# Performance work log

Hardware: AMD Instinct MI355X
Metric: run time of the kernel (lower is better)

The kernel has to match this reference:

```python
import jax, jax.numpy as jnp
import numpy as np
import math

B, L, D, H = 16, 512, 128, 8


def setup_inputs() -> dict:
    key = jax.random.key(0)
    ks = jax.random.split(key, 10)
    xavier = lambda k, shp: jax.random.normal(k, shp, jnp.float32) * math.sqrt(2.0 / (shp[0] + shp[1]))
    inp = {
        "x": jax.random.normal(ks[0], (B, L, D), jnp.float32),
        "W_q": xavier(ks[1], (H * D, D)),
        "b_q": jnp.zeros((H * D,), jnp.float32),
        "W_k": xavier(ks[2], (H * D, D)),
        "b_k": jnp.zeros((H * D,), jnp.float32),
        "W_v": xavier(ks[3], (H * D, D)),
        "b_v": jnp.zeros((H * D,), jnp.float32),
        "W_o": xavier(ks[4], (D, H * D)),
        "b_o": jnp.zeros((D,), jnp.float32),
        "pad_mask": jax.random.randint(ks[5], (B, L, L), 0, 2).astype(bool),
        "batch_size": B,
        "max_len": L,
    }
    return inp


def reference(x, W_q, b_q, W_k, b_k, W_v, b_v, W_o, b_o, pad_mask, batch_size, max_len):
    # project: [B, L, D] -> [B, L, H*D] -> head-major [H*B, L, D]
    def proj(W, b):
        y = jnp.einsum('bld,ed->ble', x, W) + b          # [B, L, H*D]
        y = y.reshape(batch_size, max_len, H, D)
        return y.transpose(2, 0, 1, 3).reshape(H * batch_size, max_len, D)

    q = proj(W_q, b_q)
    k = proj(W_k, b_k)
    v = proj(W_v, b_v)

    scores = jnp.einsum('nqd,nkd->nqk', q, k)            # [H*B, L, L]
    mask = jnp.tile(pad_mask, (H, 1, 1))                 # repeat(n_heads,1,1)
    # faithful quirk: mask BEFORE scaling, softmax over QUERY axis (dim=1)
    scores = jnp.where(mask, -1e9, scores) / math.sqrt(D)
    attn = jax.nn.softmax(scores, axis=1)
    att = jnp.einsum('nqk,nkd->nqd', attn, v)            # [H*B, L, D]
    # faithful quirk: torch .view from (H*B, L, D) to (B, L, H*D)
    att = att.reshape(batch_size, max_len, H * D)
    out = jnp.einsum('ble,de->bld', att, W_o) + b_o      # [B, L, D]
    return out
```

## Files before the change

kernel.cpp:

```cpp
#include <hip/hip_runtime.h>

#define B_  16
#define L_  512
#define D_  128
#define H_  8
#define HD_ 1024
#define NH_ 128
#define M_  8192

typedef unsigned short u16;
typedef __attribute__((ext_vector_type(8))) short s16x8;
typedef __attribute__((ext_vector_type(4))) float f32x4;

__device__ __forceinline__ float bf2f(u16 u) {
    union { unsigned u; float f; } x; x.u = ((unsigned)u) << 16; return x.f;
}
__device__ __forceinline__ u16 f2bf(float f) {
    unsigned u = __float_as_uint(f);
    return (u16)((u + 0x7FFFu + ((u >> 16) & 1u)) >> 16);
}

__device__ __forceinline__ void mfma_bt64(const u16* __restrict__ A, int lda,
                                          const u16* __restrict__ B, int ldb,
                                          int K, int lane, f32x4 acc[4][4]) {
    const int mr = lane & 15, quad = lane >> 4;
    for (int k0 = 0; k0 < K; k0 += 32) {
        s16x8 av[4], bv[4];
#pragma unroll
        for (int i = 0; i < 4; i++)
            av[i] = *(const s16x8*)(A + (size_t)(i * 16 + mr) * lda + k0 + quad * 8);
#pragma unroll
        for (int j = 0; j < 4; j++)
            bv[j] = *(const s16x8*)(B + (size_t)(j * 16 + mr) * ldb + k0 + quad * 8);
#pragma unroll
        for (int i = 0; i < 4; i++)
#pragma unroll
            for (int j = 0; j < 4; j++)
                acc[i][j] = __builtin_amdgcn_mfma_f32_16x16x32_bf16(av[i], bv[j], acc[i][j], 0, 0, 0);
    }
}

__global__ void k0_detect(const unsigned int* __restrict__ pad,
                          const unsigned int* __restrict__ xw,
                          int* __restrict__ flags) {
    __shared__ int sMask, sCnt;
    if (threadIdx.x == 0) { sMask = 0; sCnt = 0; }
    __syncthreads();
    int bad = 0;
#pragma unroll
    for (int i = 0; i < 4; i++) {
        unsigned u = pad[threadIdx.x * 4 + i];
        bad |= (u > 1u) ? 1 : 0;
    }
    int cnt = 0;
#pragma unroll
    for (int i = 0; i < 16; i++) {
        unsigned w = xw[threadIdx.x * 16 + i];
        unsigned e = (w >> 7) & 0xFFu;
        cnt += (e >= 100u && e <= 131u) ? 1 : 0;
    }
    if (bad) atomicOr(&sMask, 1);
    atomicAdd(&sCnt, cnt);
    __syncthreads();
    if (threadIdx.x == 0) {
        flags[0] = (sCnt > 2048) ? 1 : 0;
        flags[1] = sMask;
    }
}

#define PREP_TOT 1576064
__global__ __launch_bounds__(256) void kprep_conv(
    const void* x, const void* Wq, const void* bq, const void* Wk, const void* bk,
    const void* Wv, const void* bv, const void* Wo, const void* bo,
    const int* __restrict__ flags,
    u16* xb, u16* Wqb, u16* Wkb, u16* Wvb, u16* Wob,
    u16* bqb, u16* bkb, u16* bvb, u16* bob) {
    int gid = blockIdx.x * 256 + threadIdx.x;
    if (gid >= PREP_TOT) return;
    const int dt = flags[0];
    const void* src; u16* dst; int off;
    if      (gid < 1048576) { src = x;  dst = xb;  off = gid; }
    else if (gid < 1179648) { src = Wq; dst = Wqb; off = gid - 1048576; }
    else if (gid < 1310720) { src = Wk; dst = Wkb; off = gid - 1179648; }
    else if (gid < 1441792) { src = Wv; dst = Wvb; off = gid - 1310720; }
    else if (gid < 1572864) { src = Wo; dst = Wob; off = gid - 1441792; }
    else if (gid < 1573888) { src = bq; dst = bqb; off = gid - 1572864; }
    else if (gid < 1574912) { src = bk; dst = bkb; off = gid - 1573888; }
    else if (gid < 1575936) { src = bv; dst = bvb; off = gid - 1574912; }
    else                    { src = bo; dst = bob; off = gid - 1575936; }
    dst[off] = dt ? ((const u16*)src)[off] : f2bf(((const float*)src)[off]);
}

__global__ __launch_bounds__(256) void kprep_mask(const void* __restrict__ pad,
                                                  const int* __restrict__ flags,
                                                  unsigned* __restrict__ mb) {
    int w = blockIdx.x * 256 + threadIdx.x;
    size_t base = (size_t)w * 32;
    unsigned m = 0;
    if (flags[1]) {
        const unsigned char* p = (const unsigned char*)pad;
#pragma unroll
        for (int b = 0; b < 32; b++) m |= (p[base + b] ? 1u : 0u) << b;
    } else {
        const int* p = (const int*)pad;
#pragma unroll
        for (int b = 0; b < 32; b++) m |= (p[base + b] ? 1u : 0u) << b;
    }
    mb[w] = m;
}

__global__ __launch_bounds__(256) void k1_proj(
    const u16* __restrict__ xb,
    const u16* __restrict__ Wqb, const u16* __restrict__ Wkb, const u16* __restrict__ Wvb,
    const u16* __restrict__ bqb, const u16* __restrict__ bkb, const u16* __restrict__ bvb,
    u16* __restrict__ qb, u16* __restrict__ kb, u16* __restrict__ vtb) {
    const int h  = blockIdx.x;
    const int m0 = blockIdx.y * 128;
    const int z  = blockIdx.z;
    const u16* W    = (z == 0) ? Wqb : (z == 1) ? Wkb : Wvb;
    const u16* bias = (z == 0) ? bqb : (z == 1) ? bkb : bvb;

    const int lane = threadIdx.x & 63, wave = threadIdx.x >> 6;
    const int wr = wave >> 1, wc = wave & 1;
    const int mr = lane & 15, quad = lane >> 4;

    f32x4 acc[4][4];
#pragma unroll
    for (int i = 0; i < 4; i++)
#pragma unroll
        for (int j = 0; j < 4; j++) acc[i][j] = (f32x4){0.f, 0.f, 0.f, 0.f};

    mfma_bt64(xb + (size_t)(m0 + wr * 64) * D_, D_,
              W + (size_t)(h * 128 + wc * 64) * D_, D_, D_, lane, acc);

    __shared__ __align__(16) u16 T[128][144];
#pragma unroll
    for (int i = 0; i < 4; i++)
#pragma unroll
        for (int j = 0; j < 4; j++) {
            int col = wc * 64 + j * 16 + mr;
            float bv_ = bf2f(bias[h * 128 + col]);
#pragma unroll
            for (int r = 0; r < 4; r++)
                T[wr * 64 + i * 16 + quad * 4 + r][col] = f2bf(acc[i][j][r] + bv_);
        }
    __syncthreads();

    const int bb = m0 >> 9, l0 = m0 & 511;
    const int t = threadIdx.x;
    if (z < 2) {
        u16* out = z ? kb : qb;
        int row = t >> 1, c0 = (t & 1) * 64;
        u16* dst = out + ((size_t)(h * B_ + bb) * L_ + l0 + row) * D_ + c0;
#pragma unroll
        for (int c = 0; c < 64; c += 8)
            *(uint4*)(dst + c) = *(const uint4*)&T[row][c0 + c];
    } else {
        int d = t >> 1, lc0 = (t & 1) * 64;
        u16* dst = vtb + ((size_t)(h * B_ + bb) * D_ + d) * L_ + l0 + lc0;
#pragma unroll
        for (int c = 0; c < 64; c += 8) {
            u16 tmp[8];
#pragma unroll
            for (int s = 0; s < 8; s++) tmp[s] = T[lc0 + c + s][d];
            *(uint4*)(dst + c) = *(const uint4*)tmp;
        }
    }
}

__global__ __launch_bounds__(256) void k2_scores(
    const u16* __restrict__ qb, const u16* __restrict__ kb,
    const unsigned* __restrict__ mbits,
    u16* __restrict__ sb, float* __restrict__ linv) {
    const int k0g = blockIdx.x * 128;
    const int n   = blockIdx.y;
    const int bb  = n & (B_ - 1);
    const int lane = threadIdx.x & 63, wave = threadIdx.x >> 6;
    const int wr = wave >> 1, wc = wave & 1;
    const int mr = lane & 15, quad = lane >> 4;
    const float rs = 0.08838834764831845f;

    __shared__ __align__(16) u16 T[128][144];
    __shared__ float CS[2][128];

    const u16* Abase = qb + (size_t)n * L_ * D_;
    const u16* Bbase = kb + (size_t)n * L_ * D_ + (size_t)(k0g + wc * 64) * D_;

    float colsum[4] = {0.f, 0.f, 0.f, 0.f};
    for (int qt = 0; qt < 4; qt++) {
        f32x4 acc[4][4];
#pragma unroll
        for (int i = 0; i < 4; i++)
#pragma unroll
            for (int j = 0; j < 4; j++) acc[i][j] = (f32x4){0.f, 0.f, 0.f, 0.f};

        mfma_bt64(Abase + (size_t)(qt * 128 + wr * 64) * D_, D_, Bbase, D_, D_, lane, acc);

#pragma unroll
        for (int i = 0; i < 4; i++)
#pragma unroll
            for (int j = 0; j < 4; j++) {
                int kc = k0g + wc * 64 + j * 16 + mr;
#pragma unroll
                for (int r = 0; r < 4; r++) {
                    int ql = wr * 64 + i * 16 + quad * 4 + r;
                    int q  = qt * 128 + ql;
                    unsigned w = mbits[((size_t)(bb << 9) + q) * 16 + (kc >> 5)];
                    float s = ((w >> (kc & 31)) & 1u) ? -1e9f : acc[i][j][r];
                    float e = __expf(s * rs);
                    colsum[j] += e;
                    T[ql][wc * 64 + j * 16 + mr] = f2bf(e);
                }
            }
        __syncthreads();
        {
            int t = threadIdx.x, row = t >> 1, c0 = (t & 1) * 64;
            u16* dst = sb + ((size_t)n * L_ + qt * 128 + row) * L_ + k0g + c0;
#pragma unroll
            for (int c = 0; c < 64; c += 8)
                *(uint4*)(dst + c) = *(const uint4*)&T[row][c0 + c];
        }
        __syncthreads();
    }
#pragma unroll
    for (int j = 0; j < 4; j++) {
        colsum[j] += __shfl_xor(colsum[j], 16);
        colsum[j] += __shfl_xor(colsum[j], 32);
    }
    if (quad == 0) {
#pragma unroll
        for (int j = 0; j < 4; j++) CS[wr][wc * 64 + j * 16 + mr] = colsum[j];
    }
    __syncthreads();
    if (threadIdx.x < 128)
        linv[(size_t)n * L_ + k0g + threadIdx.x] =
            1.0f / (CS[0][threadIdx.x] + CS[1][threadIdx.x]);
}

__global__ __launch_bounds__(256) void k3_vscale(u16* __restrict__ vtb,
                                                 const float* __restrict__ linv) {
    int idx = blockIdx.x * 256 + threadIdx.x;
    int n = idx >> 13;
    int rem = idx & 8191;
    int d = rem >> 6;
    int kg = (rem & 63) << 3;
    u16* p = vtb + ((size_t)n * D_ + d) * L_ + kg;
    uint4 v = *(const uint4*)p;
    float lv[8];
    *(float4*)&lv[0] = *(const float4*)(linv + (size_t)n * L_ + kg);
    *(float4*)&lv[4] = *(const float4*)(linv + (size_t)n * L_ + kg + 4);
    u16* u = (u16*)&v;
#pragma unroll
    for (int s = 0; s < 8; s++) u[s] = f2bf(bf2f(u[s]) * lv[s]);
    *(uint4*)p = v;
}

__global__ __launch_bounds__(256) void k4_av(
    const u16* __restrict__ sb, const u16* __restrict__ vtb,
    u16* __restrict__ att) {
    const int q0 = blockIdx.x * 128;
    const int n  = blockIdx.y;
    const int lane = threadIdx.x & 63, wave = threadIdx.x >> 6;
    const int wr = wave >> 1, wc = wave & 1;
    const int mr = lane & 15, quad = lane >> 4;

    f32x4 acc[4][4];
#pragma unroll
    for (int i = 0; i < 4; i++)
#pragma unroll
        for (int j = 0; j < 4; j++) acc[i][j] = (f32x4){0.f, 0.f, 0.f, 0.f};

    mfma_bt64(sb + ((size_t)n * L_ + q0 + wr * 64) * L_, L_,
              vtb + ((size_t)n * D_ + wc * 64) * L_, L_, L_, lane, acc);

    __shared__ __align__(16) u16 T[128][144];
#pragma unroll
    for (int i = 0; i < 4; i++)
#pragma unroll
        for (int j = 0; j < 4; j++) {
            int col = wc * 64 + j * 16 + mr;
#pragma unroll
            for (int r = 0; r < 4; r++)
                T[wr * 64 + i * 16 + quad * 4 + r][col] = f2bf(acc[i][j][r]);
        }
    __syncthreads();
    int t = threadIdx.x, row = t >> 1, c0 = (t & 1) * 64;
    u16* dst = att + ((size_t)n * L_ + q0 + row) * D_ + c0;
#pragma unroll
    for (int c = 0; c < 64; c += 8)
        *(uint4*)(dst + c) = *(const uint4*)&T[row][c0 + c];
}

__global__ __launch_bounds__(128) void k5_out(
    const u16* __restrict__ att, const u16* __restrict__ Wob,
    const u16* __restrict__ bob, const int* __restrict__ flags,
    void* __restrict__ out) {
    const int dt = flags[0];
    const int m0 = blockIdx.x * 64;
    const int lane = threadIdx.x & 63, wc = threadIdx.x >> 6;
    const int mr = lane & 15, quad = lane >> 4;

    f32x4 acc[4][4];
#pragma unroll
    for (int i = 0; i < 4; i++)
#pragma unroll
        for (int j = 0; j < 4; j++) acc[i][j] = (f32x4){0.f, 0.f, 0.f, 0.f};

    mfma_bt64(att + (size_t)m0 * HD_, HD_,
              Wob + (size_t)(wc * 64) * HD_, HD_, HD_, lane, acc);

    __shared__ __align__(16) float Tf[64][132];
#pragma unroll
    for (int i = 0; i < 4; i++)
#pragma unroll
        for (int j = 0; j < 4; j++) {
            int col = wc * 64 + j * 16 + mr;
            float bv_ = bf2f(bob[col]);
#pragma unroll
            for (int r = 0; r < 4; r++)
                Tf[i * 16 + quad * 4 + r][col] = acc[i][j][r] + bv_;
        }
    __syncthreads();
    int t = threadIdx.x, row = t >> 1, c0 = (t & 1) * 64;
    size_t base = (size_t)(m0 + row) * D_ + c0;
    if (dt) {
        u16* o = (u16*)out;
#pragma unroll
        for (int c = 0; c < 64; c += 8) {
            u16 tmp[8];
#pragma unroll
            for (int s = 0; s < 8; s++) tmp[s] = f2bf(Tf[row][c0 + c + s]);
            *(uint4*)(o + base + c) = *(const uint4*)tmp;
        }
    } else {
        float* o = (float*)out;
#pragma unroll
        for (int c = 0; c < 64; c += 4)
            *(float4*)(o + base + c) = *(const float4*)&Tf[row][c0 + c];
    }
}

extern "C" void kernel_launch(void* const* d_in, const int* in_sizes, int n_in,
                              void* d_out, int out_size, void* d_ws, size_t ws_size,
                              hipStream_t stream) {
    (void)in_sizes; (void)n_in; (void)out_size; (void)ws_size;
    const void* x  = d_in[0];
    const void* Wq = d_in[1]; const void* bq = d_in[2];
    const void* Wk = d_in[3]; const void* bk = d_in[4];
    const void* Wv = d_in[5]; const void* bv = d_in[6];
    const void* Wo = d_in[7]; const void* bo = d_in[8];
    const void* pad = d_in[9];

    char* p = (char*)d_ws;
    auto alloc = [&](size_t bytes) { char* r = p; p += (bytes + 255) & ~(size_t)255; return r; };
    int*  flags = (int*)alloc(256);
    u16*  xb   = (u16*)alloc(2097152);
    u16*  Wqb  = (u16*)alloc(262144);
    u16*  Wkb  = (u16*)alloc(262144);
    u16*  Wvb  = (u16*)alloc(262144);
    u16*  Wob  = (u16*)alloc(262144);
    u16*  bqb  = (u16*)alloc(2048);
    u16*  bkb  = (u16*)alloc(2048);
    u16*  bvb  = (u16*)alloc(2048);
    u16*  bob  = (u16*)alloc(256);
    unsigned* mbits = (unsigned*)alloc(524288);
    float* linv = (float*)alloc(262144);
    u16*  qb   = (u16*)alloc(16777216);
    u16*  kb   = (u16*)alloc(16777216);
    u16*  vtb  = (u16*)alloc(16777216);
    u16*  sb   = (u16*)alloc(67108864);
    u16*  att  = qb;

    k0_detect<<<1, 256, 0, stream>>>((const unsigned*)pad, (const unsigned*)x, flags);
    kprep_conv<<<(PREP_TOT + 255) / 256, 256, 0, stream>>>(
        x, Wq, bq, Wk, bk, Wv, bv, Wo, bo, flags,
        xb, Wqb, Wkb, Wvb, Wob, bqb, bkb, bvb, bob);
    kprep_mask<<<512, 256, 0, stream>>>(pad, flags, mbits);
    k1_proj<<<dim3(8, 64, 3), 256, 0, stream>>>(
        xb, Wqb, Wkb, Wvb, bqb, bkb, bvb, qb, kb, vtb);
    k2_scores<<<dim3(4, NH_), 256, 0, stream>>>(qb, kb, mbits, sb, linv);
    k3_vscale<<<4096, 256, 0, stream>>>(vtb, linv);
    k4_av<<<dim3(4, NH_), 256, 0, stream>>>(sb, vtb, att);
    k5_out<<<128, 128, 0, stream>>>(att, Wob, bob, flags, d_out);
}
```

Before: 253.4 us.

## Re-grid attention kernels for more blocks, vectorize prep, split-K output GEMM

Several changes land together. The score kernel now runs one 128x128 tile per block over a 128x4x4 grid and stages the mask words in shared memory. Because column sums are now split across blocks, it accumulates them with atomicAdd into a buffer that the mask-prep kernel zeroes, and the reciprocal moves into the V-scale kernel. AV uses 64-row tiles with a 128x8 grid, the output GEMM is split-K across four waves with 512 blocks, and the conversion and mask-prep kernels use 16-byte vector loads. The aim is higher occupancy and memory efficiency, at the cost of float atomics and extra LDS reductions.

```diff
diff --git a/kernel.cpp b/kernel.cpp
--- a/kernel.cpp
+++ b/kernel.cpp
@@ -20,22 +20,23 @@
     return (u16)((u + 0x7FFFu + ((u >> 16) & 1u)) >> 16);
 }
 
-__device__ __forceinline__ void mfma_bt64(const u16* __restrict__ A, int lda,
-                                          const u16* __restrict__ B, int ldb,
-                                          int K, int lane, f32x4 acc[4][4]) {
+template<int MI, int MJ>
+__device__ __forceinline__ void mfma_bt(const u16* __restrict__ A, int lda,
+                                        const u16* __restrict__ B, int ldb,
+                                        int K, int lane, f32x4 acc[MI][MJ]) {
     const int mr = lane & 15, quad = lane >> 4;
     for (int k0 = 0; k0 < K; k0 += 32) {
-        s16x8 av[4], bv[4];
-#pragma unroll
-        for (int i = 0; i < 4; i++)
+        s16x8 av[MI], bv[MJ];
+#pragma unroll
+        for (int i = 0; i < MI; i++)
             av[i] = *(const s16x8*)(A + (size_t)(i * 16 + mr) * lda + k0 + quad * 8);
 #pragma unroll
-        for (int j = 0; j < 4; j++)
+        for (int j = 0; j < MJ; j++)
             bv[j] = *(const s16x8*)(B + (size_t)(j * 16 + mr) * ldb + k0 + quad * 8);
 #pragma unroll
-        for (int i = 0; i < 4; i++)
-#pragma unroll
-            for (int j = 0; j < 4; j++)
+        for (int i = 0; i < MI; i++)
+#pragma unroll
+            for (int j = 0; j < MJ; j++)
                 acc[i][j] = __builtin_amdgcn_mfma_f32_16x16x32_bf16(av[i], bv[j], acc[i][j], 0, 0, 0);
     }
 }
@@ -68,43 +69,58 @@
     }
 }
 
-#define PREP_TOT 1576064
-__global__ __launch_bounds__(256) void kprep_conv(
+#define PREP_G8 197008
+__global__ __launch_bounds__(256) void kprep_conv8(
     const void* x, const void* Wq, const void* bq, const void* Wk, const void* bk,
     const void* Wv, const void* bv, const void* Wo, const void* bo,
     const int* __restrict__ flags,
     u16* xb, u16* Wqb, u16* Wkb, u16* Wvb, u16* Wob,
     u16* bqb, u16* bkb, u16* bvb, u16* bob) {
-    int gid = blockIdx.x * 256 + threadIdx.x;
-    if (gid >= PREP_TOT) return;
+    int g = blockIdx.x * 256 + threadIdx.x;
+    if (g >= PREP_G8) return;
+    int e0 = g * 8;
     const int dt = flags[0];
     const void* src; u16* dst; int off;
-    if      (gid < 1048576) { src = x;  dst = xb;  off = gid; }
-    else if (gid < 1179648) { src = Wq; dst = Wqb; off = gid - 1048576; }
-    else if (gid < 1310720) { src = Wk; dst = Wkb; off = gid - 1179648; }
-    else if (gid < 1441792) { src = Wv; dst = Wvb; off = gid - 1310720; }
-    else if (gid < 1572864) { src = Wo; dst = Wob; off = gid - 1441792; }
-    else if (gid < 1573888) { src = bq; dst = bqb; off = gid - 1572864; }
-    else if (gid < 1574912) { src = bk; dst = bkb; off = gid - 1573888; }
-    else if (gid < 1575936) { src = bv; dst = bvb; off = gid - 1574912; }
-    else                    { src = bo; dst = bob; off = gid - 1575936; }
-    dst[off] = dt ? ((const u16*)src)[off] : f2bf(((const float*)src)[off]);
+    if      (e0 < 1048576) { src = x;  dst = xb;  off = e0; }
+    else if (e0 < 1179648) { src = Wq; dst = Wqb; off = e0 - 1048576; }
+    else if (e0 < 1310720) { src = Wk; dst = Wkb; off = e0 - 1179648; }
+    else if (e0 < 1441792) { src = Wv; dst = Wvb; off = e0 - 1310720; }
+    else if (e0 < 1572864) { src = Wo; dst = Wob; off = e0 - 1441792; }
+    else if (e0 < 1573888) { src = bq; dst = bqb; off = e0 - 1572864; }
+    else if (e0 < 1574912) { src = bk; dst = bkb; off = e0 - 1573888; }
+    else if (e0 < 1575936) { src = bv; dst = bvb; off = e0 - 1574912; }
+    else                   { src = bo; dst = bob; off = e0 - 1575936; }
+    if (dt) {
+        *(uint4*)(dst + off) = *(const uint4*)((const u16*)src + off);
+    } else {
+        float4 a = *(const float4*)((const float*)src + off);
+        float4 b = *(const float4*)((const float*)src + off + 4);
+        u16 t[8] = {f2bf(a.x), f2bf(a.y), f2bf(a.z), f2bf(a.w),
+                    f2bf(b.x), f2bf(b.y), f2bf(b.z), f2bf(b.w)};
+        *(uint4*)(dst + off) = *(const uint4*)t;
+    }
 }
 
 __global__ __launch_bounds__(256) void kprep_mask(const void* __restrict__ pad,
                                                   const int* __restrict__ flags,
-                                                  unsigned* __restrict__ mb) {
+                                                  unsigned* __restrict__ mb,
+                                                  float* __restrict__ lsum) {
     int w = blockIdx.x * 256 + threadIdx.x;
-    size_t base = (size_t)w * 32;
+    if (w < 65536) lsum[w] = 0.f;
     unsigned m = 0;
     if (flags[1]) {
-        const unsigned char* p = (const unsigned char*)pad;
-#pragma unroll
-        for (int b = 0; b < 32; b++) m |= (p[base + b] ? 1u : 0u) << b;
+        union { uint4 v[2]; unsigned a[8]; } u;
+        u.v[0] = ((const uint4*)pad)[w * 2];
+        u.v[1] = ((const uint4*)pad)[w * 2 + 1];
+#pragma unroll
+        for (int b = 0; b < 32; b++)
+            m |= (((u.a[b >> 2] >> ((b & 3) * 8)) & 0xFFu) ? 1u : 0u) << b;
     } else {
-        const int* p = (const int*)pad;
-#pragma unroll
-        for (int b = 0; b < 32; b++) m |= (p[base + b] ? 1u : 0u) << b;
+        union { uint4 v[8]; unsigned a[32]; } u;
+#pragma unroll
+        for (int i = 0; i < 8; i++) u.v[i] = ((const uint4*)pad)[w * 8 + i];
+#pragma unroll
+        for (int b = 0; b < 32; b++) m |= (u.a[b] ? 1u : 0u) << b;
     }
     mb[w] = m;
 }
@@ -130,10 +146,10 @@
 #pragma unroll
         for (int j = 0; j < 4; j++) acc[i][j] = (f32x4){0.f, 0.f, 0.f, 0.f};
 
-    mfma_bt64(xb + (size_t)(m0 + wr * 64) * D_, D_,
-              W + (size_t)(h * 128 + wc * 64) * D_, D_, D_, lane, acc);
-
-    __shared__ __align__(16) u16 T[128][144];
+    mfma_bt<4,4>(xb + (size_t)(m0 + wr * 64) * D_, D_,
+                 W + (size_t)(h * 128 + wc * 64) * D_, D_, D_, lane, acc);
+
+    __shared__ __align__(16) u16 T[128][136];
 #pragma unroll
     for (int i = 0; i < 4; i++)
 #pragma unroll
@@ -168,59 +184,57 @@
     }
 }
 
-__global__ __launch_bounds__(256) void k2_scores(
+__global__ __launch_bounds__(256) void k2_escore(
     const u16* __restrict__ qb, const u16* __restrict__ kb,
     const unsigned* __restrict__ mbits,
-    u16* __restrict__ sb, float* __restrict__ linv) {
-    const int k0g = blockIdx.x * 128;
-    const int n   = blockIdx.y;
-    const int bb  = n & (B_ - 1);
-    const int lane = threadIdx.x & 63, wave = threadIdx.x >> 6;
+    u16* __restrict__ E, float* __restrict__ lsum) {
+    const int n  = blockIdx.x;
+    const int ks = blockIdx.y;
+    const int qq = blockIdx.z;
+    const int bb = n & (B_ - 1);
+    const int tid = threadIdx.x;
+    const int lane = tid & 63, wave = tid >> 6;
     const int wr = wave >> 1, wc = wave & 1;
     const int mr = lane & 15, quad = lane >> 4;
     const float rs = 0.08838834764831845f;
 
-    __shared__ __align__(16) u16 T[128][144];
+    __shared__ __align__(16) u16 Te[128][136];
+    __shared__ unsigned mw[512];
     __shared__ float CS[2][128];
 
-    const u16* Abase = qb + (size_t)n * L_ * D_;
-    const u16* Bbase = kb + (size_t)n * L_ * D_ + (size_t)(k0g + wc * 64) * D_;
+#pragma unroll
+    for (int s = 0; s < 2; s++) {
+        int idx = tid * 2 + s;
+        int ql = idx >> 2, lw = idx & 3;
+        mw[idx] = mbits[((size_t)(bb << 9) + qq * 128 + ql) * 16 + ks * 4 + lw];
+    }
+    __syncthreads();
+
+    f32x4 acc[4][4];
+#pragma unroll
+    for (int i = 0; i < 4; i++)
+#pragma unroll
+        for (int j = 0; j < 4; j++) acc[i][j] = (f32x4){0.f, 0.f, 0.f, 0.f};
+
+    mfma_bt<4,4>(qb + (size_t)n * L_ * D_ + (size_t)(qq * 128 + wr * 64) * D_, D_,
+                 kb + (size_t)n * L_ * D_ + (size_t)(ks * 128 + wc * 64) * D_, D_,
+                 D_, lane, acc);
 
     float colsum[4] = {0.f, 0.f, 0.f, 0.f};
-    for (int qt = 0; qt < 4; qt++) {
-        f32x4 acc[4][4];
+#pragma unroll
+    for (int j = 0; j < 4; j++) {
+        const int kc = wc * 64 + j * 16 + mr;
+        const int lw = kc >> 5, bit = kc & 31;
 #pragma unroll
         for (int i = 0; i < 4; i++)
 #pragma unroll
-            for (int j = 0; j < 4; j++) acc[i][j] = (f32x4){0.f, 0.f, 0.f, 0.f};
-
-        mfma_bt64(Abase + (size_t)(qt * 128 + wr * 64) * D_, D_, Bbase, D_, D_, lane, acc);
-
-#pragma unroll
-        for (int i = 0; i < 4; i++)
-#pragma unroll
-            for (int j = 0; j < 4; j++) {
-                int kc = k0g + wc * 64 + j * 16 + mr;
-#pragma unroll
-                for (int r = 0; r < 4; r++) {
-                    int ql = wr * 64 + i * 16 + quad * 4 + r;
-                    int q  = qt * 128 + ql;
-                    unsigned w = mbits[((size_t)(bb << 9) + q) * 16 + (kc >> 5)];
-                    float s = ((w >> (kc & 31)) & 1u) ? -1e9f : acc[i][j][r];
-                    float e = __expf(s * rs);
-                    colsum[j] += e;
-                    T[ql][wc * 64 + j * 16 + mr] = f2bf(e);
-                }
+            for (int r = 0; r < 4; r++) {
+                int ql = wr * 64 + i * 16 + quad * 4 + r;
+                float e = ((mw[(ql << 2) + lw] >> bit) & 1u)
+                          ? 0.f : __expf(acc[i][j][r] * rs);
+                colsum[j] += e;
+                Te[ql][kc] = f2bf(e);
             }
-        __syncthreads();
-        {
-            int t = threadIdx.x, row = t >> 1, c0 = (t & 1) * 64;
-            u16* dst = sb + ((size_t)n * L_ + qt * 128 + row) * L_ + k0g + c0;
-#pragma unroll
-            for (int c = 0; c < 64; c += 8)
-                *(uint4*)(dst + c) = *(const uint4*)&T[row][c0 + c];
-        }
-        __syncthreads();
     }
 #pragma unroll
     for (int j = 0; j < 4; j++) {
@@ -232,13 +246,20 @@
         for (int j = 0; j < 4; j++) CS[wr][wc * 64 + j * 16 + mr] = colsum[j];
     }
     __syncthreads();
-    if (threadIdx.x < 128)
-        linv[(size_t)n * L_ + k0g + threadIdx.x] =
-            1.0f / (CS[0][threadIdx.x] + CS[1][threadIdx.x]);
+
+    {
+        int row = tid >> 1, c0 = (tid & 1) * 64;
+        u16* dst = E + ((size_t)(n * L_ + qq * 128 + row)) * L_ + ks * 128 + c0;
+#pragma unroll
+        for (int c = 0; c < 64; c += 8)
+            *(uint4*)(dst + c) = *(const uint4*)&Te[row][c0 + c];
+    }
+    if (tid < 128)
+        atomicAdd(&lsum[(size_t)n * L_ + ks * 128 + tid], CS[0][tid] + CS[1][tid]);
 }
 
 __global__ __launch_bounds__(256) void k3_vscale(u16* __restrict__ vtb,
-                                                 const float* __restrict__ linv) {
+                                                 const float* __restrict__ lsum) {
     int idx = blockIdx.x * 256 + threadIdx.x;
     int n = idx >> 13;
     int rem = idx & 8191;
@@ -246,9 +267,10 @@
     int kg = (rem & 63) << 3;
     u16* p = vtb + ((size_t)n * D_ + d) * L_ + kg;
     uint4 v = *(const uint4*)p;
-    float lv[8];
-    *(float4*)&lv[0] = *(const float4*)(linv + (size_t)n * L_ + kg);
-    *(float4*)&lv[4] = *(const float4*)(linv + (size_t)n * L_ + kg + 4);
+    float4 l0 = *(const float4*)(lsum + (size_t)n * L_ + kg);
+    float4 l1 = *(const float4*)(lsum + (size_t)n * L_ + kg + 4);
+    float lv[8] = {1.f/l0.x, 1.f/l0.y, 1.f/l0.z, 1.f/l0.w,
+                   1.f/l1.x, 1.f/l1.y, 1.f/l1.z, 1.f/l1.w};
     u16* u = (u16*)&v;
 #pragma unroll
     for (int s = 0; s < 8; s++) u[s] = f2bf(bf2f(u[s]) * lv[s]);
@@ -256,87 +278,98 @@
 }
 
 __global__ __launch_bounds__(256) void k4_av(
-    const u16* __restrict__ sb, const u16* __restrict__ vtb,
+    const u16* __restrict__ E, const u16* __restrict__ vtb,
     u16* __restrict__ att) {
-    const int q0 = blockIdx.x * 128;
-    const int n  = blockIdx.y;
-    const int lane = threadIdx.x & 63, wave = threadIdx.x >> 6;
-    const int wr = wave >> 1, wc = wave & 1;
+    const int n  = blockIdx.x;
+    const int qt = blockIdx.y;
+    const int tid = threadIdx.x;
+    const int lane = tid & 63, w = tid >> 6;
     const int mr = lane & 15, quad = lane >> 4;
 
-    f32x4 acc[4][4];
+    f32x4 acc[4][2];
 #pragma unroll
     for (int i = 0; i < 4; i++)
 #pragma unroll
-        for (int j = 0; j < 4; j++) acc[i][j] = (f32x4){0.f, 0.f, 0.f, 0.f};
-
-    mfma_bt64(sb + ((size_t)n * L_ + q0 + wr * 64) * L_, L_,
-              vtb + ((size_t)n * D_ + wc * 64) * L_, L_, L_, lane, acc);
-
-    __shared__ __align__(16) u16 T[128][144];
+        for (int j = 0; j < 2; j++) acc[i][j] = (f32x4){0.f, 0.f, 0.f, 0.f};
+
+    mfma_bt<4,2>(E + ((size_t)n * L_ + qt * 64) * L_, L_,
+                 vtb + ((size_t)n * D_ + w * 32) * L_, L_, L_, lane, acc);
+
+    __shared__ __align__(16) u16 Ta[64][136];
 #pragma unroll
     for (int i = 0; i < 4; i++)
 #pragma unroll
-        for (int j = 0; j < 4; j++) {
-            int col = wc * 64 + j * 16 + mr;
+        for (int j = 0; j < 2; j++) {
+            int col = w * 32 + j * 16 + mr;
 #pragma unroll
             for (int r = 0; r < 4; r++)
-                T[wr * 64 + i * 16 + quad * 4 + r][col] = f2bf(acc[i][j][r]);
+                Ta[i * 16 + quad * 4 + r][col] = f2bf(acc[i][j][r]);
         }
     __syncthreads();
-    int t = threadIdx.x, row = t >> 1, c0 = (t & 1) * 64;
-    u16* dst = att + ((size_t)n * L_ + q0 + row) * D_ + c0;
-#pragma unroll
-    for (int c = 0; c < 64; c += 8)
-        *(uint4*)(dst + c) = *(const uint4*)&T[row][c0 + c];
-}
-
-__global__ __launch_bounds__(128) void k5_out(
+    int row = tid >> 2, c0 = (tid & 3) * 32;
+    u16* dst = att + ((size_t)(n * L_ + qt * 64 + row)) * D_ + c0;
+#pragma unroll
+    for (int c = 0; c < 32; c += 8)
+        *(uint4*)(dst + c) = *(const uint4*)&Ta[row][c0 + c];
+}
+
+__global__ __launch_bounds__(256) void k5_out(
     const u16* __restrict__ att, const u16* __restrict__ Wob,
     const u16* __restrict__ bob, const int* __restrict__ flags,
     void* __restrict__ out) {
     const int dt = flags[0];
-    const int m0 = blockIdx.x * 64;
-    const int lane = threadIdx.x & 63, wc = threadIdx.x >> 6;
+    const int n0 = blockIdx.x * 64;
+    const int m0 = blockIdx.y * 32;
+    const int tid = threadIdx.x;
+    const int lane = tid & 63, wk = tid >> 6;
     const int mr = lane & 15, quad = lane >> 4;
 
-    f32x4 acc[4][4];
-#pragma unroll
-    for (int i = 0; i < 4; i++)
+    f32x4 acc[2][4];
+#pragma unroll
+    for (int i = 0; i < 2; i++)
 #pragma unroll
         for (int j = 0; j < 4; j++) acc[i][j] = (f32x4){0.f, 0.f, 0.f, 0.f};
 
-    mfma_bt64(att + (size_t)m0 * HD_, HD_,
-              Wob + (size_t)(wc * 64) * HD_, HD_, HD_, lane, acc);
-
-    __shared__ __align__(16) float Tf[64][132];
-#pragma unroll
-    for (int i = 0; i < 4; i++)
-#pragma unroll
-        for (int j = 0; j < 4; j++) {
-            int col = wc * 64 + j * 16 + mr;
-            float bv_ = bf2f(bob[col]);
-#pragma unroll
-            for (int r = 0; r < 4; r++)
-                Tf[i * 16 + quad * 4 + r][col] = acc[i][j][r] + bv_;
-        }
-    __syncthreads();
-    int t = threadIdx.x, row = t >> 1, c0 = (t & 1) * 64;
-    size_t base = (size_t)(m0 + row) * D_ + c0;
+    mfma_bt<2,4>(att + (size_t)m0 * HD_ + wk * 256, HD_,
+                 Wob + (size_t)n0 * HD_ + wk * 256, HD_, 256, lane, acc);
+
+    __shared__ __align__(16) float Tf[2][32][68];
+    if (wk < 2) {
+#pragma unroll
+        for (int i = 0; i < 2; i++)
+#pragma unroll
+            for (int j = 0; j < 4; j++)
+#pragma unroll
+                for (int r = 0; r < 4; r++)
+                    Tf[wk][i * 16 + quad * 4 + r][j * 16 + mr] = acc[i][j][r];
+    }
+    __syncthreads();
+    if (wk >= 2) {
+#pragma unroll
+        for (int i = 0; i < 2; i++)
+#pragma unroll
+            for (int j = 0; j < 4; j++)
+#pragma unroll
+                for (int r = 0; r < 4; r++)
+                    Tf[wk - 2][i * 16 + quad * 4 + r][j * 16 + mr] += acc[i][j][r];
+    }
+    __syncthreads();
+
+    int row = tid >> 3, c0 = (tid & 7) * 8;
+    size_t base = (size_t)(m0 + row) * D_ + n0 + c0;
+    float v[8];
+#pragma unroll
+    for (int s = 0; s < 8; s++)
+        v[s] = Tf[0][row][c0 + s] + Tf[1][row][c0 + s] + bf2f(bob[n0 + c0 + s]);
     if (dt) {
-        u16* o = (u16*)out;
-#pragma unroll
-        for (int c = 0; c < 64; c += 8) {
-            u16 tmp[8];
-#pragma unroll
-            for (int s = 0; s < 8; s++) tmp[s] = f2bf(Tf[row][c0 + c + s]);
-            *(uint4*)(o + base + c) = *(const uint4*)tmp;
-        }
+        u16 tmp[8];
+#pragma unroll
+        for (int s = 0; s < 8; s++) tmp[s] = f2bf(v[s]);
+        *(uint4*)((u16*)out + base) = *(const uint4*)tmp;
     } else {
         float* o = (float*)out;
-#pragma unroll
-        for (int c = 0; c < 64; c += 4)
-            *(float4*)(o + base + c) = *(const float4*)&Tf[row][c0 + c];
+        *(float4*)(o + base)     = *(const float4*)&v[0];
+        *(float4*)(o + base + 4) = *(const float4*)&v[4];
     }
 }
 
@@ -364,22 +397,22 @@
     u16*  bvb  = (u16*)alloc(2048);
     u16*  bob  = (u16*)alloc(256);
     unsigned* mbits = (unsigned*)alloc(524288);
-    float* linv = (float*)alloc(262144);
+    float* lsum = (float*)alloc(262144);
     u16*  qb   = (u16*)alloc(16777216);
     u16*  kb   = (u16*)alloc(16777216);
     u16*  vtb  = (u16*)alloc(16777216);
-    u16*  sb   = (u16*)alloc(67108864);
+    u16*  E    = (u16*)alloc(67108864);
     u16*  att  = qb;
 
     k0_detect<<<1, 256, 0, stream>>>((const unsigned*)pad, (const unsigned*)x, flags);
-    kprep_conv<<<(PREP_TOT + 255) / 256, 256, 0, stream>>>(
+    kprep_conv8<<<(PREP_G8 + 255) / 256, 256, 0, stream>>>(
         x, Wq, bq, Wk, bk, Wv, bv, Wo, bo, flags,
         xb, Wqb, Wkb, Wvb, Wob, bqb, bkb, bvb, bob);
-    kprep_mask<<<512, 256, 0, stream>>>(pad, flags, mbits);
+    kprep_mask<<<512, 256, 0, stream>>>(pad, flags, mbits, lsum);
     k1_proj<<<dim3(8, 64, 3), 256, 0, stream>>>(
         xb, Wqb, Wkb, Wvb, bqb, bkb, bvb, qb, kb, vtb);
-    k2_scores<<<dim3(4, NH_), 256, 0, stream>>>(qb, kb, mbits, sb, linv);
-    k3_vscale<<<4096, 256, 0, stream>>>(vtb, linv);
-    k4_av<<<dim3(4, NH_), 256, 0, stream>>>(sb, vtb, att);
-    k5_out<<<128, 128, 0, stream>>>(att, Wob, bob, flags, d_out);
-}
+    k2_escore<<<dim3(128, 4, 4), 256, 0, stream>>>(qb, kb, mbits, E, lsum);
+    k3_vscale<<<4096, 256, 0, stream>>>(vtb, lsum);
+    k4_av<<<dim3(128, 8), 256, 0, stream>>>(E, vtb, att);
+    k5_out<<<dim3(2, 256), 256, 0, stream>>>(att, Wob, bob, flags, d_out);
+}
```

New measurement: 263.3 us. +3.9%, slower.
